# Performance work log

Hardware: AMD Instinct MI355X
Metric: run time of the kernel (lower is better)

Reference implementation:

```python
import jax, jax.numpy as jnp
import numpy as np

K = 16  # neighbors per patchlet (init default)


def _gather(points, idx):
    # points: (b, n, c), idx: (b, m, k) -> (b, m, k, c)  (per-batch gather, = utils.index_points)
    return jax.vmap(lambda p, i: p[i])(points, idx)


def setup_inputs() -> dict:
    key = jax.random.key(0)
    point_seq = jax.random.normal(key, (8, 32, 1024, 3), dtype=jnp.float32)  # (b, t, n, 3)
    return {"point_seq": point_seq}


def reference(point_seq):
    b, t, n, d = point_seq.shape
    k = K
    # feat_seq is None in this config -> features are the points themselves
    feat_seq = point_seq
    # feat_seq_2 = cat([feat[:, [0]], feat], 1)[:, :-1]  (previous frame's feats, first frame repeated)
    feat_prev_seq = jnp.concatenate([feat_seq[:, :1], feat_seq[:, :-1]], axis=1)

    # scan over time: carry = tracked centroids x_current (b, n, 3)
    xs = (jnp.swapaxes(point_seq, 0, 1), jnp.swapaxes(feat_prev_seq, 0, 1))  # (t, b, n, .)
    x0 = point_seq[:, 0]  # x2[:, 0]

    def step(x_cur, inp):
        x_next, feat_prev = inp  # (b, n, 3), (b, n, 3)
        # brute-force squared-distance kNN (== keops Kmin_argKmin, ascending)
        q2 = jnp.sum(x_cur * x_cur, axis=-1)[:, :, None]      # (b, n, 1)
        p2 = jnp.sum(x_next * x_next, axis=-1)[:, None, :]    # (b, 1, n)
        d2 = q2 + p2 - 2.0 * jnp.einsum('bqd,bpd->bqp', x_cur, x_next)  # (b, n, n)
        neg_d, idxs = jax.lax.top_k(-d2, k)                   # smallest-k, ascending
        dist = -neg_d                                          # (b, n, k)
        pts = _gather(x_next, idxs)                            # (b, n, k, 3)
        feats = _gather(feat_prev, idxs)                       # (b, n, k, 3)
        x_new = pts[:, :, 0, :]                                # sample_mode == 'nn'
        return x_new, (dist, idxs, pts, feats, x_new)

    _, (dist, idxs, pts, feats, outx) = jax.lax.scan(step, x0, xs)

    # (t, b, ...) -> (b, t, ...)
    dist = jnp.swapaxes(dist, 0, 1)
    idxs = jnp.swapaxes(idxs, 0, 1)
    pts = jnp.swapaxes(pts, 0, 1)          # patchlet_points (b, t, n, k, 3)
    feats = jnp.swapaxes(feats, 0, 1)      # (b, t, n, k, 3)
    outx = jnp.swapaxes(outx, 0, 1)        # x_current (b, t, n, 3)

    # normalize by first-frame anchor point (detached in torch)
    anchor = jax.lax.stop_gradient(pts[:, :1, :, :1, :])  # (b, 1, n, 1, 3)
    normalized = pts - anchor
    patchlet_feats = jnp.concatenate([feats, normalized], axis=-1)  # (b, t, n, k, 6)

    # (idx, distances, patchlets, patchlet_points, patchlet_feats, normalized_patchlet_points, x_current)
    return (idxs, dist, idxs, pts, patchlet_feats, normalized, outx)
```

## Files before the change

kernel.cpp:

```cpp
#include <hip/hip_runtime.h>
#include <stdint.h>

#define NB 8
#define NT 32
#define NN 1024
#define KSEL 16

typedef unsigned long long u64;
typedef unsigned int u32;

#define O_IDX0 0ull
#define O_DIST 4194304ull
#define O_IDX1 8388608ull
#define O_PTS  12582912ull
#define O_PF   25165824ull
#define O_NORM 50331648ull
#define O_OUTX 62914560ull

#define F32_INF __uint_as_float(0x7F800000u)
#define MARGIN 1e-3f

__device__ __forceinline__ u32 fmap(float f) {
    u32 b = __float_as_uint(f);
    u32 m = (u32)((int)b >> 31) | 0x80000000u;
    return b ^ m;
}
__device__ __forceinline__ float sq3(float x, float y, float z) {
    return __fmaf_rn(z, z, __fmaf_rn(x, x, __fmul_rn(y, y)));
}
__device__ __forceinline__ float d2f(float qx, float qy, float qz, float q2, float4 c) {
    float dot = __fmul_rn(qx, c.x);
    dot = __fmaf_rn(qy, c.y, dot);
    dot = __fmaf_rn(qz, c.z, dot);
    return __fsub_rn(__fadd_rn(q2, c.w), __fadd_rn(dot, dot));
}

#define INSERT16(D2V, JV)                                                        \
{                                                                                \
    _Pragma("unroll")                                                            \
    for (int s = KSEL - 1; s >= 1; --s) {                                        \
        ID[s] = ((D2V) < K[s - 1]) ? ID[s - 1] : (((D2V) < K[s]) ? (JV) : ID[s]);\
        K[s]  = __builtin_fminf(__builtin_fmaxf((D2V), K[s - 1]), K[s]);         \
    }                                                                            \
    ID[0] = ((D2V) < K[0]) ? (JV) : ID[0];                                       \
    K[0]  = __builtin_fminf((D2V), K[0]);                                        \
}

__global__ __launch_bounds__(256) void chain_k(const float* __restrict__ P,
                                               float* __restrict__ outx) {
    __shared__ float4 sF[NN];
    const int tid = threadIdx.x;
    const int bid = blockIdx.x;
    const int b = bid >> 7;
    const int qb = (bid & 127) << 3;
    const int ln = tid & 63;
    const int q = qb + ((tid >> 6) << 1) + (ln >> 5);
    const int sl = ln & 31;
    const float* bp = P + (size_t)b * NT * NN * 3;

    float cx = bp[q * 3 + 0], cy = bp[q * 3 + 1], cz = bp[q * 3 + 2];

    for (int t = 0; t < NT; ++t) {
        const float4* f4 = (const float4*)(bp + (size_t)t * NN * 3);
        float4 A = f4[tid * 3 + 0], Bv = f4[tid * 3 + 1], C = f4[tid * 3 + 2];
        sF[tid * 4 + 0] = make_float4(A.x, A.y, A.z, sq3(A.x, A.y, A.z));
        sF[tid * 4 + 1] = make_float4(A.w, Bv.x, Bv.y, sq3(A.w, Bv.x, Bv.y));
        sF[tid * 4 + 2] = make_float4(Bv.z, Bv.w, C.x, sq3(Bv.z, Bv.w, C.x));
        sF[tid * 4 + 3] = make_float4(C.y, C.z, C.w, sq3(C.y, C.z, C.w));
        __syncthreads();

        float q2 = sq3(cx, cy, cz);
        float bd = F32_INF;
        u32 bj = 0u;
        #pragma unroll 8
        for (int i = 0; i < 32; ++i) {
            int j = (i << 5) | sl;
            float d2 = d2f(cx, cy, cz, q2, sF[j]);
            bool c_ = d2 < bd;
            bd = c_ ? d2 : bd;
            bj = c_ ? (u32)j : bj;
        }
        u64 key = ((u64)fmap(bd) << 32) | (u64)bj;
        #pragma unroll
        for (int off = 1; off < 32; off <<= 1) {
            u64 o = __shfl_xor(key, off);
            key = (o < key) ? o : key;
        }
        int bi = (int)((u32)key & 1023u);
        float4 w = sF[bi];
        cx = w.x; cy = w.y; cz = w.z;
        if (sl == 0) {
            float* o = outx + ((size_t)(b * NT + t) * NN + q) * 3;
            o[0] = cx; o[1] = cy; o[2] = cz;
        }
        __syncthreads();
    }
}

__global__ __launch_bounds__(256, 4) void topk_k(const float* __restrict__ P,
                                                 const float* __restrict__ outx,
                                                 float* __restrict__ out) {
    __shared__ float4 sC[NN];
    __shared__ float4 sPv[NN];
    const int tid = threadIdx.x;
    const int bid = blockIdx.x;
    const int b = bid >> 7;
    const int t = (bid >> 2) & 31;
    const int qc = bid & 3;
    const int q = (qc << 8) | tid;
    const float* bp = P + (size_t)b * NT * NN * 3;

    {
        const float4* f4 = (const float4*)(bp + (size_t)t * NN * 3);
        float4 A = f4[tid * 3 + 0], Bv = f4[tid * 3 + 1], C = f4[tid * 3 + 2];
        sC[tid * 4 + 0] = make_float4(A.x, A.y, A.z, sq3(A.x, A.y, A.z));
        sC[tid * 4 + 1] = make_float4(A.w, Bv.x, Bv.y, sq3(A.w, Bv.x, Bv.y));
        sC[tid * 4 + 2] = make_float4(Bv.z, Bv.w, C.x, sq3(Bv.z, Bv.w, C.x));
        sC[tid * 4 + 3] = make_float4(C.y, C.z, C.w, sq3(C.y, C.z, C.w));
        int tp = (t == 0) ? 0 : (t - 1);
        const float4* g4 = (const float4*)(bp + (size_t)tp * NN * 3);
        A = g4[tid * 3 + 0]; Bv = g4[tid * 3 + 1]; C = g4[tid * 3 + 2];
        sPv[tid * 4 + 0] = make_float4(A.x, A.y, A.z, 0.f);
        sPv[tid * 4 + 1] = make_float4(A.w, Bv.x, Bv.y, 0.f);
        sPv[tid * 4 + 2] = make_float4(Bv.z, Bv.w, C.x, 0.f);
        sPv[tid * 4 + 3] = make_float4(C.y, C.z, C.w, 0.f);
    }
    __syncthreads();

    float cx, cy, cz;
    if (t == 0) {
        const float* qp = bp + (size_t)q * 3;
        cx = qp[0]; cy = qp[1]; cz = qp[2];
    } else {
        const float* qp = outx + ((size_t)(b * NT + (t - 1)) * NN + q) * 3;
        cx = qp[0]; cy = qp[1]; cz = qp[2];
    }
    const float* ap = outx + ((size_t)(b * NT) * NN + q) * 3;
    float ax = ap[0], ay = ap[1], az = ap[2];

    float q2 = sq3(cx, cy, cz);
    float K[KSEL];
    u32 ID[KSEL];
    #pragma unroll
    for (int i = 0; i < KSEL; i++) { K[i] = F32_INF; ID[i] = 0u; }

    for (u32 j = 0; j < 32; ++j) {
        float d2 = d2f(cx, cy, cz, q2, sC[j]);
        INSERT16(d2, j)
    }
    float thr = K[KSEL - 1];

    for (int ch = 1; ch < 32; ++ch) {
        float thrq = __fadd_rn(__fsub_rn(thr, q2), MARGIN);
        u32 m = 0u;
        #pragma unroll
        for (int jj = 0; jj < 32; ++jj) {
            float4 c = sC[(ch << 5) | jj];
            float dt = __fmaf_rn(c.z, cz, __fmaf_rn(c.y, cy, __fmul_rn(c.x, cx)));
            float lhs = __fmaf_rn(-2.0f, dt, c.w);
            m |= (lhs < thrq) ? (1u << jj) : 0u;
        }
        int cm = __popc(m);
        #pragma unroll
        for (int off = 1; off < 64; off <<= 1) {
            int o = __shfl_xor(cm, off);
            cm = (o > cm) ? o : cm;
        }
        cm = __builtin_amdgcn_readfirstlane(cm);
        for (int i = 0; i < cm; ++i) {
            bool act = m != 0u;
            u32 mm = act ? m : 1u;
            u32 jj = (u32)__builtin_ctz(mm);
            m &= (m - 1u);
            u32 j = (u32)(ch << 5) | jj;
            float4 c = sC[j];
            float d2 = d2f(cx, cy, cz, q2, c);
            float d2v = act ? d2 : F32_INF;
            INSERT16(d2v, j)
        }
        thr = K[KSEL - 1];
    }

    size_t g = (size_t)(b * NT + t) * NN + q;

    #pragma unroll
    for (int kk = 0; kk < KSEL; kk += 4) {
        float4 fi = make_float4((float)ID[kk + 0], (float)ID[kk + 1],
                                (float)ID[kk + 2], (float)ID[kk + 3]);
        float4 fd = make_float4(K[kk + 0], K[kk + 1], K[kk + 2], K[kk + 3]);
        *(float4*)(out + O_IDX0 + g * 16 + kk) = fi;
        *(float4*)(out + O_IDX1 + g * 16 + kk) = fi;
        *(float4*)(out + O_DIST + g * 16 + kk) = fd;
    }

    #pragma unroll
    for (int kk = 0; kk < KSEL; kk += 4) {
        u32 i0 = ID[kk + 0], i1 = ID[kk + 1], i2 = ID[kk + 2], i3 = ID[kk + 3];
        float4 p0 = sC[i0], p1 = sC[i1], p2v = sC[i2], p3 = sC[i3];
        float4 f0 = sPv[i0], f1 = sPv[i1], f2v = sPv[i2], f3 = sPv[i3];
        float n0x = p0.x - ax, n0y = p0.y - ay, n0z = p0.z - az;
        float n1x = p1.x - ax, n1y = p1.y - ay, n1z = p1.z - az;
        float n2x = p2v.x - ax, n2y = p2v.y - ay, n2z = p2v.z - az;
        float n3x = p3.x - ax, n3y = p3.y - ay, n3z = p3.z - az;

        float* pp = out + O_PTS + g * 48 + kk * 3;
        ((float4*)pp)[0] = make_float4(p0.x, p0.y, p0.z, p1.x);
        ((float4*)pp)[1] = make_float4(p1.y, p1.z, p2v.x, p2v.y);
        ((float4*)pp)[2] = make_float4(p2v.z, p3.x, p3.y, p3.z);

        float* np = out + O_NORM + g * 48 + kk * 3;
        ((float4*)np)[0] = make_float4(n0x, n0y, n0z, n1x);
        ((float4*)np)[1] = make_float4(n1y, n1z, n2x, n2y);
        ((float4*)np)[2] = make_float4(n2z, n3x, n3y, n3z);

        float* fp = out + O_PF + g * 96 + kk * 6;
        ((float4*)fp)[0] = make_float4(f0.x, f0.y, f0.z, n0x);
        ((float4*)fp)[1] = make_float4(n0y, n0z, f1.x, f1.y);
        ((float4*)fp)[2] = make_float4(f1.z, n1x, n1y, n1z);
        ((float4*)fp)[3] = make_float4(f2v.x, f2v.y, f2v.z, n2x);
        ((float4*)fp)[4] = make_float4(n2y, n2z, f3.x, f3.y);
        ((float4*)fp)[5] = make_float4(f3.z, n3x, n3y, n3z);
    }
}

extern "C" void kernel_launch(void* const* d_in, const int* in_sizes, int n_in,
                              void* d_out, int out_size, void* d_ws, size_t ws_size,
                              hipStream_t stream) {
    const float* P = (const float*)d_in[0];
    float* out = (float*)d_out;
    float* outx = out + O_OUTX;
    chain_k<<<dim3(1024), dim3(256), 0, stream>>>(P, outx);
    topk_k<<<dim3(1024), dim3(256), 0, stream>>>(P, outx, out);
}
```

Before: 442.4 us.

## Split kNN selection into a value-only pass and an index-collection pass

The top-16 search now first tracks only distance values, using a cheaper insertion network without index bookkeeping, over 64-wide chunks with an exact threshold test instead of a margin. A second full scan then writes every index whose distance is within the final 16th value into a per-thread FIFO in shared memory. A last short insertion pass rebuilds sorted indices from that FIFO. The aim is to cut the index-select work in the hot insertion loop, at the price of an extra full distance pass, one LDS store per point, and truncation if ties overflow the 32-entry FIFO.

```diff
diff --git a/kernel.cpp b/kernel.cpp
--- a/kernel.cpp
+++ b/kernel.cpp
@@ -5,6 +5,7 @@
 #define NT 32
 #define NN 1024
 #define KSEL 16
+#define FIFODEPTH 32
 
 typedef unsigned long long u64;
 typedef unsigned int u32;
@@ -18,7 +19,6 @@
 #define O_OUTX 62914560ull
 
 #define F32_INF __uint_as_float(0x7F800000u)
-#define MARGIN 1e-3f
 
 __device__ __forceinline__ u32 fmap(float f) {
     u32 b = __float_as_uint(f);
@@ -33,6 +33,14 @@
     dot = __fmaf_rn(qy, c.y, dot);
     dot = __fmaf_rn(qz, c.z, dot);
     return __fsub_rn(__fadd_rn(q2, c.w), __fadd_rn(dot, dot));
+}
+
+#define INSERTK(D2V)                                                             \
+{                                                                                \
+    _Pragma("unroll")                                                            \
+    for (int s = KSEL - 1; s >= 1; --s)                                          \
+        K[s] = __builtin_fminf(__builtin_fmaxf((D2V), K[s - 1]), K[s]);          \
+    K[0] = __builtin_fminf((D2V), K[0]);                                         \
 }
 
 #define INSERT16(D2V, JV)                                                        \
@@ -102,6 +110,7 @@
                                                  float* __restrict__ out) {
     __shared__ float4 sC[NN];
     __shared__ float4 sPv[NN];
+    __shared__ unsigned short sQ[FIFODEPTH * 256];
     const int tid = threadIdx.x;
     const int bid = blockIdx.x;
     const int b = bid >> 7;
@@ -140,27 +149,27 @@
 
     float q2 = sq3(cx, cy, cz);
     float K[KSEL];
-    u32 ID[KSEL];
-    #pragma unroll
-    for (int i = 0; i < KSEL; i++) { K[i] = F32_INF; ID[i] = 0u; }
-
-    for (u32 j = 0; j < 32; ++j) {
+    #pragma unroll
+    for (int i = 0; i < KSEL; i++) K[i] = F32_INF;
+
+    #pragma unroll 8
+    for (u32 j = 0; j < 64; ++j) {
         float d2 = d2f(cx, cy, cz, q2, sC[j]);
-        INSERT16(d2, j)
+        INSERTK(d2)
     }
     float thr = K[KSEL - 1];
 
-    for (int ch = 1; ch < 32; ++ch) {
-        float thrq = __fadd_rn(__fsub_rn(thr, q2), MARGIN);
-        u32 m = 0u;
-        #pragma unroll
-        for (int jj = 0; jj < 32; ++jj) {
-            float4 c = sC[(ch << 5) | jj];
-            float dt = __fmaf_rn(c.z, cz, __fmaf_rn(c.y, cy, __fmul_rn(c.x, cx)));
-            float lhs = __fmaf_rn(-2.0f, dt, c.w);
-            m |= (lhs < thrq) ? (1u << jj) : 0u;
-        }
-        int cm = __popc(m);
+    for (int ch = 1; ch < 16; ++ch) {
+        u32 mlo = 0u, mhi = 0u;
+        #pragma unroll
+        for (int jj = 0; jj < 64; ++jj) {
+            float d2 = d2f(cx, cy, cz, q2, sC[(ch << 6) | jj]);
+            bool h = d2 < thr;
+            if (jj < 32) mlo |= h ? (1u << jj) : 0u;
+            else         mhi |= h ? (1u << (jj - 32)) : 0u;
+        }
+        u64 msk = ((u64)mhi << 32) | (u64)mlo;
+        int cm = __builtin_popcountll(msk);
         #pragma unroll
         for (int off = 1; off < 64; off <<= 1) {
             int o = __shfl_xor(cm, off);
@@ -168,17 +177,48 @@
         }
         cm = __builtin_amdgcn_readfirstlane(cm);
         for (int i = 0; i < cm; ++i) {
-            bool act = m != 0u;
-            u32 mm = act ? m : 1u;
-            u32 jj = (u32)__builtin_ctz(mm);
-            m &= (m - 1u);
-            u32 j = (u32)(ch << 5) | jj;
-            float4 c = sC[j];
-            float d2 = d2f(cx, cy, cz, q2, c);
+            bool act = msk != 0ull;
+            u64 mm = act ? msk : 1ull;
+            u32 jj = (u32)__builtin_ctzll(mm);
+            msk &= (msk - 1ull);
+            float d2 = d2f(cx, cy, cz, q2, sC[(ch << 6) | jj]);
             float d2v = act ? d2 : F32_INF;
-            INSERT16(d2v, j)
+            INSERTK(d2v)
         }
         thr = K[KSEL - 1];
+    }
+
+    const float K15f = K[KSEL - 1];
+    int cnt = 0;
+    for (int ch = 0; ch < 16; ++ch) {
+        #pragma unroll
+        for (int jj = 0; jj < 64; ++jj) {
+            u32 j = ((u32)ch << 6) | (u32)jj;
+            float d2 = d2f(cx, cy, cz, q2, sC[j]);
+            bool h = d2 <= K15f;
+            int slot = (cnt < FIFODEPTH - 1) ? cnt : (FIFODEPTH - 1);
+            sQ[slot * 256 + tid] = (unsigned short)j;
+            cnt += h ? 1 : 0;
+        }
+    }
+    if (cnt > FIFODEPTH) cnt = FIFODEPTH;
+
+    u32 ID[KSEL];
+    #pragma unroll
+    for (int i = 0; i < KSEL; i++) { K[i] = F32_INF; ID[i] = 0u; }
+    int cm = cnt;
+    #pragma unroll
+    for (int off = 1; off < 64; off <<= 1) {
+        int o = __shfl_xor(cm, off);
+        cm = (o > cm) ? o : cm;
+    }
+    cm = __builtin_amdgcn_readfirstlane(cm);
+    for (int i = 0; i < cm; ++i) {
+        u32 j = (u32)sQ[i * 256 + tid] & 1023u;
+        float4 c = sC[j];
+        float d2 = d2f(cx, cy, cz, q2, c);
+        float d2v = (i < cnt) ? d2 : F32_INF;
+        INSERT16(d2v, j)
     }
 
     size_t g = (size_t)(b * NT + t) * NN + q;
```

New measurement: 496.3 us. +12.2%, slower.

## Widen top-k filter chunks to 64, use exact d2 filter and med3 insert

Applied to the files above, without the earlier changes.

The top-k kernel now runs 512-thread blocks over 512 queries each, so every block stages shared memory once for twice as many queries. It filters 64 candidates per chunk with a 64-bit mask, compares the exact squared distance against the threshold instead of a margin-relaxed form, and builds the sorted insert with fmed3. Larger chunks mean fewer wave-wide max reductions and threshold refreshes, but more candidates may survive per chunk and the 64-iteration seed costs more. The block count is halved, and register pressure under the (512,6) launch bounds could spill.

```diff
diff --git a/kernel.cpp b/kernel.cpp
--- a/kernel.cpp
+++ b/kernel.cpp
@@ -18,7 +18,12 @@
 #define O_OUTX 62914560ull
 
 #define F32_INF __uint_as_float(0x7F800000u)
-#define MARGIN 1e-3f
+
+#if __has_builtin(__builtin_amdgcn_fmed3f)
+#define MED3(X, A, B) __builtin_amdgcn_fmed3f((X), (A), (B))
+#else
+#define MED3(X, A, B) __builtin_fminf(__builtin_fmaxf((X), (A)), (B))
+#endif
 
 __device__ __forceinline__ u32 fmap(float f) {
     u32 b = __float_as_uint(f);
@@ -40,7 +45,7 @@
     _Pragma("unroll")                                                            \
     for (int s = KSEL - 1; s >= 1; --s) {                                        \
         ID[s] = ((D2V) < K[s - 1]) ? ID[s - 1] : (((D2V) < K[s]) ? (JV) : ID[s]);\
-        K[s]  = __builtin_fminf(__builtin_fmaxf((D2V), K[s - 1]), K[s]);         \
+        K[s]  = MED3((D2V), K[s - 1], K[s]);                                     \
     }                                                                            \
     ID[0] = ((D2V) < K[0]) ? (JV) : ID[0];                                       \
     K[0]  = __builtin_fminf((D2V), K[0]);                                        \
@@ -97,33 +102,35 @@
     }
 }
 
-__global__ __launch_bounds__(256, 4) void topk_k(const float* __restrict__ P,
+__global__ __launch_bounds__(512, 6) void topk_k(const float* __restrict__ P,
                                                  const float* __restrict__ outx,
                                                  float* __restrict__ out) {
     __shared__ float4 sC[NN];
     __shared__ float4 sPv[NN];
     const int tid = threadIdx.x;
     const int bid = blockIdx.x;
-    const int b = bid >> 7;
-    const int t = (bid >> 2) & 31;
-    const int qc = bid & 3;
-    const int q = (qc << 8) | tid;
+    const int b = bid >> 6;
+    const int t = (bid >> 1) & 31;
+    const int qc = bid & 1;
+    const int q = (qc << 9) | tid;
     const float* bp = P + (size_t)b * NT * NN * 3;
 
-    {
+    if (tid < 256) {
         const float4* f4 = (const float4*)(bp + (size_t)t * NN * 3);
         float4 A = f4[tid * 3 + 0], Bv = f4[tid * 3 + 1], C = f4[tid * 3 + 2];
         sC[tid * 4 + 0] = make_float4(A.x, A.y, A.z, sq3(A.x, A.y, A.z));
         sC[tid * 4 + 1] = make_float4(A.w, Bv.x, Bv.y, sq3(A.w, Bv.x, Bv.y));
         sC[tid * 4 + 2] = make_float4(Bv.z, Bv.w, C.x, sq3(Bv.z, Bv.w, C.x));
         sC[tid * 4 + 3] = make_float4(C.y, C.z, C.w, sq3(C.y, C.z, C.w));
-        int tp = (t == 0) ? 0 : (t - 1);
+    } else {
+        const int t2 = tid - 256;
+        const int tp = (t == 0) ? 0 : (t - 1);
         const float4* g4 = (const float4*)(bp + (size_t)tp * NN * 3);
-        A = g4[tid * 3 + 0]; Bv = g4[tid * 3 + 1]; C = g4[tid * 3 + 2];
-        sPv[tid * 4 + 0] = make_float4(A.x, A.y, A.z, 0.f);
-        sPv[tid * 4 + 1] = make_float4(A.w, Bv.x, Bv.y, 0.f);
-        sPv[tid * 4 + 2] = make_float4(Bv.z, Bv.w, C.x, 0.f);
-        sPv[tid * 4 + 3] = make_float4(C.y, C.z, C.w, 0.f);
+        float4 A = g4[t2 * 3 + 0], Bv = g4[t2 * 3 + 1], C = g4[t2 * 3 + 2];
+        sPv[t2 * 4 + 0] = make_float4(A.x, A.y, A.z, 0.f);
+        sPv[t2 * 4 + 1] = make_float4(A.w, Bv.x, Bv.y, 0.f);
+        sPv[t2 * 4 + 2] = make_float4(Bv.z, Bv.w, C.x, 0.f);
+        sPv[t2 * 4 + 3] = make_float4(C.y, C.z, C.w, 0.f);
     }
     __syncthreads();
 
@@ -144,23 +151,23 @@
     #pragma unroll
     for (int i = 0; i < KSEL; i++) { K[i] = F32_INF; ID[i] = 0u; }
 
-    for (u32 j = 0; j < 32; ++j) {
+    for (u32 j = 0; j < 64; ++j) {
         float d2 = d2f(cx, cy, cz, q2, sC[j]);
         INSERT16(d2, j)
     }
     float thr = K[KSEL - 1];
 
-    for (int ch = 1; ch < 32; ++ch) {
-        float thrq = __fadd_rn(__fsub_rn(thr, q2), MARGIN);
-        u32 m = 0u;
+    for (int ch = 1; ch < 16; ++ch) {
+        u32 mlo = 0u, mhi = 0u;
         #pragma unroll
-        for (int jj = 0; jj < 32; ++jj) {
-            float4 c = sC[(ch << 5) | jj];
-            float dt = __fmaf_rn(c.z, cz, __fmaf_rn(c.y, cy, __fmul_rn(c.x, cx)));
-            float lhs = __fmaf_rn(-2.0f, dt, c.w);
-            m |= (lhs < thrq) ? (1u << jj) : 0u;
-        }
-        int cm = __popc(m);
+        for (int jj = 0; jj < 64; ++jj) {
+            float d2 = d2f(cx, cy, cz, q2, sC[(ch << 6) | jj]);
+            bool h = d2 < thr;
+            if (jj < 32) mlo |= h ? (1u << jj) : 0u;
+            else         mhi |= h ? (1u << (jj - 32)) : 0u;
+        }
+        u64 msk = ((u64)mhi << 32) | (u64)mlo;
+        int cm = __builtin_popcountll(msk);
         #pragma unroll
         for (int off = 1; off < 64; off <<= 1) {
             int o = __shfl_xor(cm, off);
@@ -168,11 +175,11 @@
         }
         cm = __builtin_amdgcn_readfirstlane(cm);
         for (int i = 0; i < cm; ++i) {
-            bool act = m != 0u;
-            u32 mm = act ? m : 1u;
-            u32 jj = (u32)__builtin_ctz(mm);
-            m &= (m - 1u);
-            u32 j = (u32)(ch << 5) | jj;
+            bool act = msk != 0ull;
+            u64 mm = act ? msk : 1ull;
+            u32 jj = (u32)__builtin_ctzll(mm);
+            msk &= (msk - 1ull);
+            u32 j = ((u32)ch << 6) | jj;
             float4 c = sC[j];
             float d2 = d2f(cx, cy, cz, q2, c);
             float d2v = act ? d2 : F32_INF;
@@ -230,5 +237,5 @@
     float* out = (float*)d_out;
     float* outx = out + O_OUTX;
     chain_k<<<dim3(1024), dim3(256), 0, stream>>>(P, outx);
-    topk_k<<<dim3(1024), dim3(256), 0, stream>>>(P, outx, out);
-}
+    topk_k<<<dim3(512), dim3(512), 0, stream>>>(P, outx, out);
+}
```

Measured after the change: 484.2 us. 9.4% more time.
